# Performance work log

Hardware: AMD Instinct MI355X
Metric: run time of the kernel (lower is better)

The kernel has to match this reference:

```python
import jax, jax.numpy as jnp
import numpy as np

N, H, T, L, D_IN, D_QK, D_V = 8, 8, 1024, 1024, 128, 128, 128


def setup_inputs() -> dict:
    key = jax.random.key(0)
    ks = jax.random.split(key, 12)
    s = 1.0 / np.sqrt(D_IN)
    sq = 1.0 / np.sqrt(D_QK)
    return {
        "X": jax.random.normal(ks[0], (N, H, L, D_IN), jnp.float32),
        "t1": jax.random.normal(ks[1], (N, T), jnp.float32),
        "Q": jax.random.normal(ks[2], (N, H, T, D_QK), jnp.float32),
        "Wk1": jax.random.normal(ks[3], (D_IN, D_QK), jnp.float32) * s,
        "bk1": jnp.zeros((D_QK,), jnp.float32),
        "Wk2": jax.random.normal(ks[4], (D_QK, D_QK), jnp.float32) * sq,
        "bk2": jnp.zeros((D_QK,), jnp.float32),
        "Wv1": jax.random.normal(ks[5], (D_IN, D_QK), jnp.float32) * s,
        "bv1": jnp.zeros((D_QK,), jnp.float32),
        "Wv2": jax.random.normal(ks[6], (D_QK, D_V), jnp.float32) * sq,
        "bv2": jnp.zeros((D_V,), jnp.float32),
        "log_tau": jnp.asarray(0.0, jnp.float32),  # log(init_tau=1)
    }


def _mlp(x, W1, b1, W2, b2):
    # MLP(d_in, [d_qk], d_out): Linear -> relu -> Linear
    return jax.nn.relu(x @ W1 + b1) @ W2 + b2


def reference(X, t1, Q, Wk1, bk1, Wk2, bk2, Wv1, bv1, Wv2, bv2, log_tau):
    t2 = X[:, 0, :, -1]                      # (N, L)
    K = _mlp(X, Wk1, bk1, Wk2, bk2)          # (N, H, L, d_qk)
    V = _mlp(X, Wv1, bv1, Wv2, bv2)          # (N, H, L, d_v)
    tau = jnp.exp(log_tau)
    # gaussian weight: -(Q.K)^2 / tau
    A = jnp.einsum('nhtc,nhlc->nhtl', Q, K)
    A = -(A * A) / tau
    mask = (t1[:, :, None] >= t2[:, None, :])[:, None, :, :]  # (N,1,T,L)
    A = jax.nn.softmax(A * mask, axis=-1) * mask
    return jnp.einsum('nhtl,nhlc->nhtc', A, V)
```

## Files before the change

### kernel.cpp

```cpp
#include <hip/hip_runtime.h>
#include <hip/hip_bf16.h>

typedef __bf16 bf16_t;
typedef _Float16 f16_t;
typedef bf16_t bf16x8 __attribute__((ext_vector_type(8)));
typedef f16_t  f16x8  __attribute__((ext_vector_type(8)));
typedef float  floatx4 __attribute__((ext_vector_type(4)));
typedef bf16x8 bf16x8u __attribute__((aligned(8)));

#define DEV static __device__ __forceinline__

DEV floatx4 mfma_bf16(bf16x8 a, bf16x8 b, floatx4 c) {
  return __builtin_amdgcn_mfma_f32_16x16x32_bf16(a, b, c, 0, 0, 0);
}
DEV floatx4 mfma_f16(f16x8 a, f16x8 b, floatx4 c) {
  return __builtin_amdgcn_mfma_f32_16x16x32_f16(a, b, c, 0, 0, 0);
}
DEV void async_ld16(void* lds, const void* g) {
  __builtin_amdgcn_global_load_lds(
      (const __attribute__((address_space(1))) unsigned int*)g,
      (__attribute__((address_space(3))) unsigned int*)lds, 16, 0, 0);
}

__global__ void prep_kernel(const float* __restrict__ Wk1, const float* __restrict__ Wk2,
                            const float* __restrict__ Wv1, const float* __restrict__ Wv2,
                            const float* __restrict__ X,
                            bf16_t* __restrict__ W1p, bf16_t* __restrict__ W2p,
                            f16_t* __restrict__ W1f, f16_t* __restrict__ W2f,
                            float* __restrict__ t2pre) {
  int b = blockIdx.x;
  if (b < 16) {
    int m = b >> 2, p = b & 3;
    const float* src = m == 0 ? Wk1 : m == 1 ? Wk2 : m == 2 ? Wv1 : Wv2;
    for (int u = 0; u < 16; ++u) {
      int idx = p * 4096 + u * 256 + threadIdx.x;
      int k = idx >> 7, nn = idx & 127;
      float v = src[idx];
      int o = nn * 128 + k;
      if (m == 0) { bf16_t h = (bf16_t)v; W1p[o] = h; W1p[16384 + o] = (bf16_t)(v - (float)h); }
      else if (m == 1) { bf16_t h = (bf16_t)v; W2p[o] = h; W2p[16384 + o] = (bf16_t)(v - (float)h); }
      else if (m == 2) W1f[o] = (f16_t)v;
      else W2f[o] = (f16_t)v;
    }
  } else {
    int i = (b - 16) * 256 + threadIdx.x;
    t2pre[i] = X[((size_t)(i >> 10) * 8192 + (i & 1023)) * 128 + 127];
  }
}

__global__ __launch_bounds__(256) void mlp_k_kernel(
    const float* __restrict__ X, const float* __restrict__ b1,
    const float* __restrict__ b2, const bf16_t* __restrict__ W1p,
    const bf16_t* __restrict__ W2p, bf16_t* __restrict__ Khi,
    bf16_t* __restrict__ Klo) {
  __shared__ __align__(16) bf16_t sXh[64 * 132];
  __shared__ __align__(16) bf16_t sXl[64 * 132];
  __shared__ __align__(16) bf16_t sW[256 * 40];

  const int tid = threadIdx.x, lane = tid & 63, wave = tid >> 6;
  const int q = lane >> 4, c15 = lane & 15;
  const size_t rowBase = (size_t)blockIdx.x * 64;
  const floatx4 FZ = {0.f, 0.f, 0.f, 0.f};

  int goff[5];
  for (int a = 0; a < 5; ++a) {
    int o = (wave + 4 * a) * 1024 + lane * 16;
    int row = o / 80, rem = o % 80;
    goff[a] = row * 256 + (rem < 64 ? rem : 0);
  }
  float b1v[8], b2v[8];
  for (int nt = 0; nt < 8; ++nt) { b1v[nt] = b1[nt * 16 + c15]; b2v[nt] = b2[nt * 16 + c15]; }

  for (int u = 0; u < 8; ++u) {
    int idx = tid + u * 256;
    int r = idx >> 5, c4 = (idx & 31) << 2;
    float4 v = *(const float4*)(X + (rowBase + r) * 128 + c4);
    int o = r * 132 + c4;
    float vv[4] = {v.x, v.y, v.z, v.w};
    for (int i = 0; i < 4; ++i) {
      bf16_t h = (bf16_t)vv[i];
      sXh[o + i] = h;
      sXl[o + i] = (bf16_t)(vv[i] - (float)h);
    }
  }

  auto issueW = [&](const bf16_t* Wp, int kq) {
    const char* base = (const char*)Wp + kq * 64;
    for (int a = 0; a < 5; ++a)
      async_ld16((char*)sW + (wave + 4 * a) * 1024 + lane * 16, base + goff[a]);
  };
  auto gemm = [&](const bf16_t* Wp, floatx4* acc, bool first) {
    for (int kq = 0; kq < 4; ++kq) {
      if (!first || kq) __syncthreads();
      issueW(Wp, kq);
      __syncthreads();
      const int ao = (wave * 16 + c15) * 132 + kq * 32 + q * 8;
      bf16x8 ah = *(const bf16x8u*)(sXh + ao);
      bf16x8 al = *(const bf16x8u*)(sXl + ao);
      for (int nt = 0; nt < 8; ++nt) {
        const int bo = (nt * 16 + c15) * 40 + q * 8;
        bf16x8 bh = *(const bf16x8*)(sW + bo);
        bf16x8 bl = *(const bf16x8*)(sW + 128 * 40 + bo);
        acc[nt] = mfma_bf16(ah, bh, acc[nt]);
        acc[nt] = mfma_bf16(ah, bl, acc[nt]);
        acc[nt] = mfma_bf16(al, bh, acc[nt]);
      }
    }
  };

  floatx4 acc1[8];
  for (int i = 0; i < 8; ++i) acc1[i] = FZ;
  gemm(W1p, acc1, true);

  for (int nt = 0; nt < 8; ++nt)
    for (int r = 0; r < 4; ++r) {
      float h = fmaxf(acc1[nt][r] + b1v[nt], 0.f);
      bf16_t hh = (bf16_t)h;
      int o = (wave * 16 + q * 4 + r) * 132 + nt * 16 + c15;
      sXh[o] = hh;
      sXl[o] = (bf16_t)(h - (float)hh);
    }

  floatx4 acc2[8];
  for (int i = 0; i < 8; ++i) acc2[i] = FZ;
  gemm(W2p, acc2, false);

  for (int nt = 0; nt < 8; ++nt)
    for (int r = 0; r < 4; ++r) {
      float kv = acc2[nt][r] + b2v[nt];
      bf16_t kh = (bf16_t)kv;
      int o = (wave * 16 + q * 4 + r) * 132 + nt * 16 + c15;
      sXh[o] = kh;
      sXl[o] = (bf16_t)(kv - (float)kh);
    }
  __syncthreads();
  for (int u = 0; u < 4; ++u) {
    int idx = tid + u * 256;
    int r = idx >> 4, c8 = (idx & 15) << 3;
    bf16x8 vh = *(const bf16x8u*)(sXh + r * 132 + c8);
    bf16x8 vl = *(const bf16x8u*)(sXl + r * 132 + c8);
    *(bf16x8*)(Khi + (rowBase + r) * 128 + c8) = vh;
    *(bf16x8*)(Klo + (rowBase + r) * 128 + c8) = vl;
  }
}

__global__ __launch_bounds__(256) void mlp_v_kernel(
    const float* __restrict__ X, const float* __restrict__ b1,
    const float* __restrict__ b2, const f16_t* __restrict__ W1f,
    const f16_t* __restrict__ W2f, f16_t* __restrict__ Vt) {
  __shared__ __align__(16) f16_t sXf[9216];
  __shared__ __align__(16) f16_t sW[128 * 40];

  const int tid = threadIdx.x, lane = tid & 63, wave = tid >> 6;
  const int q = lane >> 4, c15 = lane & 15;
  const size_t rowBase = (size_t)blockIdx.x * 64;
  const floatx4 FZ = {0.f, 0.f, 0.f, 0.f};

  int goff[3];
  for (int a = 0; a < 3; ++a) {
    int j = wave + 4 * a;
    int o = j * 1024 + lane * 16;
    int row = o / 80, rem = o % 80;
    goff[a] = row * 256 + (rem < 64 ? rem : 0);
  }
  float b1v[8], bvv[2][4];
  for (int nt = 0; nt < 8; ++nt) b1v[nt] = b1[nt * 16 + c15];
  for (int mt = 0; mt < 2; ++mt)
    for (int r = 0; r < 4; ++r)
      bvv[mt][r] = b2[(wave * 2 + mt) * 16 + q * 4 + r];

  for (int u = 0; u < 8; ++u) {
    int idx = tid + u * 256;
    int r = idx >> 5, c4 = (idx & 31) << 2;
    float4 v = *(const float4*)(X + (rowBase + r) * 128 + c4);
    int o = r * 136 + c4;
    sXf[o + 0] = (f16_t)v.x; sXf[o + 1] = (f16_t)v.y;
    sXf[o + 2] = (f16_t)v.z; sXf[o + 3] = (f16_t)v.w;
  }

  auto issueV = [&](const f16_t* Wp, int kq) {
    const char* base = (const char*)Wp + kq * 64;
    for (int a = 0; a < 3; ++a) {
      int j = wave + 4 * a;
      if (j < 10) async_ld16((char*)sW + j * 1024 + lane * 16, base + goff[a]);
    }
  };

  floatx4 acc1[8];
  for (int i = 0; i < 8; ++i) acc1[i] = FZ;
  for (int kq = 0; kq < 4; ++kq) {
    if (kq) __syncthreads();
    issueV(W1f, kq);
    __syncthreads();
    f16x8 a = *(const f16x8*)(sXf + (wave * 16 + c15) * 136 + kq * 32 + q * 8);
    for (int nt = 0; nt < 8; ++nt) {
      f16x8 bb = *(const f16x8*)(sW + (nt * 16 + c15) * 40 + q * 8);
      acc1[nt] = mfma_f16(a, bb, acc1[nt]);
    }
  }
  for (int nt = 0; nt < 8; ++nt)
    for (int r = 0; r < 4; ++r)
      sXf[(wave * 16 + q * 4 + r) * 136 + nt * 16 + c15] =
          (f16_t)fmaxf(acc1[nt][r] + b1v[nt], 0.f);

  floatx4 acc2[2][4];
  for (int i = 0; i < 2; ++i) for (int j = 0; j < 4; ++j) acc2[i][j] = FZ;
  for (int kq = 0; kq < 4; ++kq) {
    __syncthreads();
    issueV(W2f, kq);
    __syncthreads();
    f16x8 aw0 = *(const f16x8*)(sW + ((wave * 2 + 0) * 16 + c15) * 40 + q * 8);
    f16x8 aw1 = *(const f16x8*)(sW + ((wave * 2 + 1) * 16 + c15) * 40 + q * 8);
    for (int nt = 0; nt < 4; ++nt) {
      f16x8 bh = *(const f16x8*)(sXf + (nt * 16 + c15) * 136 + kq * 32 + q * 8);
      acc2[0][nt] = mfma_f16(aw0, bh, acc2[0][nt]);
      acc2[1][nt] = mfma_f16(aw1, bh, acc2[1][nt]);
    }
  }
  __syncthreads();
  for (int mt = 0; mt < 2; ++mt)
    for (int nt = 0; nt < 4; ++nt)
      for (int r = 0; r < 4; ++r) {
        int c = (wave * 2 + mt) * 16 + q * 4 + r;
        sXf[c * 72 + nt * 16 + c15] = (f16_t)(acc2[mt][nt][r] + bvv[mt][r]);
      }
  __syncthreads();
  const int nh = (int)(rowBase >> 10);
  const int lB = (int)(rowBase & 1023);
  for (int u = 0; u < 4; ++u) {
    int idx = tid + u * 256;
    int c = idx >> 3, l8 = (idx & 7) << 3;
    *(f16x8*)(Vt + ((size_t)nh * 128 + c) * 1024 + lB + l8) =
        *(const f16x8*)(sXf + c * 72 + l8);
  }
}

__global__ __launch_bounds__(256) void attn_kernel(
    const float* __restrict__ Q, const float* __restrict__ t1,
    const float* __restrict__ t2pre, const float* __restrict__ ltau,
    const bf16_t* __restrict__ Khi, const bf16_t* __restrict__ Klo,
    const f16_t* __restrict__ Vt, float* __restrict__ out) {
  __shared__ __align__(16) char sBuf[2][27648];
  __shared__ __align__(16) f16_t sP[128 * 40];

  const int tid = threadIdx.x, lane = tid & 63, wave = tid >> 6;
  const int q = lane >> 4, c15 = lane & 15;
  const int nh = blockIdx.x & 63;
  const int tB = (blockIdx.x >> 6) << 7;
  const int n = nh >> 3;
  const float c2 = __expf(-ltau[0]) * 1.44269504f;
  const floatx4 FZ = {0.f, 0.f, 0.f, 0.f};

  const char* gp[7]; int ls[7]; int st[7];
  for (int a = 0; a < 7; ++a) {
    int j = wave + 4 * a;
    gp[a] = nullptr; ls[a] = 0; st[a] = 0;
    if (j < 17) {
      int o = j * 1024 + lane * 16;
      int half = o >= 8704 ? 1 : 0;
      int r2 = o - half * 8704;
      int row = r2 / 272, rem = r2 % 272;
      if (rem >= 256) rem = 0;
      gp[a] = (const char*)(half ? Klo : Khi) + ((size_t)((nh << 10) + row)) * 256 + rem;
      st[a] = 8192; ls[a] = o;
    } else if (j < 27) {
      int o = (j - 17) * 1024 + lane * 16;
      int c = o / 80, rem = o % 80;
      if (rem >= 64) rem = 0;
      gp[a] = (const char*)Vt + ((size_t)((nh << 7) + c)) * 2048 + rem;
      st[a] = 64; ls[a] = 17408 + o;
    }
  }
  auto stage = [&](int buf) {
    for (int a = 0; a < 7; ++a) {
      int j = wave + 4 * a;
      if (j < 27) { async_ld16(sBuf[buf] + ls[a], gp[a]); gp[a] += st[a]; }
    }
  };

  bf16x8 qh[2][4], ql[2][4];
  for (int mt = 0; mt < 2; ++mt) {
    int t = tB + (wave * 2 + mt) * 16 + c15;
    const float* qr = Q + ((size_t)(nh << 10) + t) * 128;
    for (int kc = 0; kc < 4; ++kc) {
      const float* p = qr + kc * 32 + q * 8;
      float4 v0 = *(const float4*)p;
      float4 v1 = *(const float4*)(p + 4);
      float vv[8] = {v0.x, v0.y, v0.z, v0.w, v1.x, v1.y, v1.z, v1.w};
      bf16x8 h, l;
      for (int j = 0; j < 8; ++j) {
        bf16_t hj = (bf16_t)vv[j];
        h[j] = hj;
        l[j] = (bf16_t)(vv[j] - (float)hj);
      }
      qh[mt][kc] = h;
      ql[mt][kc] = l;
    }
  }
  float t1v[2][4];
  for (int mt = 0; mt < 2; ++mt)
    for (int r = 0; r < 4; ++r)
      t1v[mt][r] = t1[(n << 10) + tB + (wave * 2 + mt) * 16 + q * 4 + r];
  const float* t2p = t2pre + (n << 10);

  floatx4 O[2][8];
  for (int i = 0; i < 2; ++i) for (int j = 0; j < 8; ++j) O[i][j] = FZ;
  float ds[2][4] = {{0.f, 0.f, 0.f, 0.f}, {0.f, 0.f, 0.f, 0.f}};

  stage(0);
  __syncthreads();
  for (int it = 0; it < 32; ++it) {
    const int cur = it & 1;
    if (it < 31) stage(cur ^ 1);
    float t2a = t2p[c15], t2b = t2p[c15 + 16];
    t2p += 32;
    const bf16_t* kb = (const bf16_t*)sBuf[cur];
    const f16_t* vb = (const f16_t*)(sBuf[cur] + 17408);

    floatx4 S[2][2];
    S[0][0] = FZ; S[0][1] = FZ; S[1][0] = FZ; S[1][1] = FZ;
    for (int nt = 0; nt < 2; ++nt)
      for (int kc = 0; kc < 4; ++kc) {
        int bo = (nt * 16 + c15) * 136 + kc * 32 + q * 8;
        bf16x8 bh = *(const bf16x8*)(kb + bo);
        bf16x8 bl = *(const bf16x8*)(kb + 4352 + bo);
        for (int mt = 0; mt < 2; ++mt) {
          S[mt][nt] = mfma_bf16(qh[mt][kc], bh, S[mt][nt]);
          S[mt][nt] = mfma_bf16(qh[mt][kc], bl, S[mt][nt]);
          S[mt][nt] = mfma_bf16(ql[mt][kc], bh, S[mt][nt]);
        }
      }
    for (int mt = 0; mt < 2; ++mt)
      for (int nt = 0; nt < 2; ++nt) {
        float t2v = nt ? t2b : t2a;
        for (int r = 0; r < 4; ++r) {
          float s = S[mt][nt][r];
          float e = exp2f(-s * s * c2);
          bool m = (t1v[mt][r] >= t2v);
          ds[mt][r] += m ? e : 1.f;
          sP[((wave * 2 + mt) * 16 + q * 4 + r) * 40 + nt * 16 + c15] =
              (f16_t)(m ? e : 0.f);
        }
      }
    f16x8 ap[2];
    for (int mt = 0; mt < 2; ++mt)
      ap[mt] = *(const f16x8*)(sP + ((wave * 2 + mt) * 16 + c15) * 40 + q * 8);
    for (int ct = 0; ct < 8; ++ct) {
      f16x8 bv = *(const f16x8*)(vb + (ct * 16 + c15) * 40 + q * 8);
      for (int mt = 0; mt < 2; ++mt)
        O[mt][ct] = mfma_f16(ap[mt], bv, O[mt][ct]);
    }
    __syncthreads();
  }

  for (int mt = 0; mt < 2; ++mt)
    for (int r = 0; r < 4; ++r) {
      float v = ds[mt][r];
      v += __shfl_xor(v, 1);
      v += __shfl_xor(v, 2);
      v += __shfl_xor(v, 4);
      v += __shfl_xor(v, 8);
      ds[mt][r] = 1.f / v;
    }
  for (int mt = 0; mt < 2; ++mt) {
    int rowb = tB + (wave * 2 + mt) * 16 + q * 4;
    for (int ct = 0; ct < 8; ++ct)
      for (int r = 0; r < 4; ++r)
        out[((size_t)(nh << 10) + rowb + r) * 128 + ct * 16 + c15] =
            O[mt][ct][r] * ds[mt][r];
  }
}

extern "C" void kernel_launch(void* const* d_in, const int* in_sizes, int n_in,
                              void* d_out, int out_size, void* d_ws, size_t ws_size,
                              hipStream_t stream) {
  const float* X   = (const float*)d_in[0];
  const float* t1  = (const float*)d_in[1];
  const float* Q   = (const float*)d_in[2];
  const float* Wk1 = (const float*)d_in[3];
  const float* bk1 = (const float*)d_in[4];
  const float* Wk2 = (const float*)d_in[5];
  const float* bk2 = (const float*)d_in[6];
  const float* Wv1 = (const float*)d_in[7];
  const float* bv1 = (const float*)d_in[8];
  const float* Wv2 = (const float*)d_in[9];
  const float* bv2 = (const float*)d_in[10];
  const float* log_tau = (const float*)d_in[11];
  float* out = (float*)d_out;

  const size_t E = (size_t)64 * 1024 * 128;
  bf16_t* Khi = (bf16_t*)d_ws;
  bf16_t* Klo = Khi + E;
  f16_t*  Vt  = (f16_t*)(Klo + E);
  bf16_t* W1p = (bf16_t*)((char*)d_ws + 3 * E * 2);
  bf16_t* W2p = W1p + 32768;
  f16_t*  W1f = (f16_t*)(W2p + 32768);
  f16_t*  W2f = W1f + 16384;
  float*  t2pre = (float*)(W2f + 16384);

  prep_kernel<<<48, 256, 0, stream>>>(Wk1, Wk2, Wv1, Wv2, X, W1p, W2p, W1f, W2f, t2pre);
  mlp_k_kernel<<<1024, 256, 0, stream>>>(X, bk1, bk2, W1p, W2p, Khi, Klo);
  mlp_v_kernel<<<1024, 256, 0, stream>>>(X, bv1, bv2, W1f, W2f, Vt);
  attn_kernel<<<512, 256, 0, stream>>>(Q, t1, t2pre, log_tau, Khi, Klo, Vt, out);
}
```

Measured before the change: 242.8 us.

## Rework attention to 32x32 MFMA and double-buffer MLP weights with split-bf16 V path

The attention kernel now uses 32x32 MFMA tiles, with one query row per lane. The softmax probabilities are fed straight from registers into the PV MFMA, which removes the sP shared-memory round trip and its layout. t2 is staged in LDS once, and the kernel declares a launch bound of two blocks per CU. Both MLP kernels double-buffer the weight tiles across the two GEMM phases to drop a barrier per step. The V MLP switches from fp16 to three-pass split bf16 for accuracy, which adds MFMA work and larger LDS use.

```diff
diff --git a/kernel.cpp b/kernel.cpp
--- a/kernel.cpp
+++ b/kernel.cpp
@@ -5,16 +5,21 @@
 typedef _Float16 f16_t;
 typedef bf16_t bf16x8 __attribute__((ext_vector_type(8)));
 typedef f16_t  f16x8  __attribute__((ext_vector_type(8)));
+typedef f16_t  f16x4  __attribute__((ext_vector_type(4)));
 typedef float  floatx4 __attribute__((ext_vector_type(4)));
+typedef float  floatx16 __attribute__((ext_vector_type(16)));
 typedef bf16x8 bf16x8u __attribute__((aligned(8)));
 
 #define DEV static __device__ __forceinline__
 
-DEV floatx4 mfma_bf16(bf16x8 a, bf16x8 b, floatx4 c) {
+DEV floatx4 mfma16_bf16(bf16x8 a, bf16x8 b, floatx4 c) {
   return __builtin_amdgcn_mfma_f32_16x16x32_bf16(a, b, c, 0, 0, 0);
 }
-DEV floatx4 mfma_f16(f16x8 a, f16x8 b, floatx4 c) {
-  return __builtin_amdgcn_mfma_f32_16x16x32_f16(a, b, c, 0, 0, 0);
+DEV floatx16 mfma32_bf16(bf16x8 a, bf16x8 b, floatx16 c) {
+  return __builtin_amdgcn_mfma_f32_32x32x16_bf16(a, b, c, 0, 0, 0);
+}
+DEV floatx16 mfma32x8_f16(f16x4 a, f16x4 b, floatx16 c) {
+  return __builtin_amdgcn_mfma_f32_32x32x8f16(a, b, c, 0, 0, 0);
 }
 DEV void async_ld16(void* lds, const void* g) {
   __builtin_amdgcn_global_load_lds(
@@ -26,21 +31,21 @@
                             const float* __restrict__ Wv1, const float* __restrict__ Wv2,
                             const float* __restrict__ X,
                             bf16_t* __restrict__ W1p, bf16_t* __restrict__ W2p,
-                            f16_t* __restrict__ W1f, f16_t* __restrict__ W2f,
+                            bf16_t* __restrict__ W3p, bf16_t* __restrict__ W4p,
                             float* __restrict__ t2pre) {
   int b = blockIdx.x;
   if (b < 16) {
     int m = b >> 2, p = b & 3;
     const float* src = m == 0 ? Wk1 : m == 1 ? Wk2 : m == 2 ? Wv1 : Wv2;
+    bf16_t* dst = m == 0 ? W1p : m == 1 ? W2p : m == 2 ? W3p : W4p;
     for (int u = 0; u < 16; ++u) {
       int idx = p * 4096 + u * 256 + threadIdx.x;
       int k = idx >> 7, nn = idx & 127;
       float v = src[idx];
       int o = nn * 128 + k;
-      if (m == 0) { bf16_t h = (bf16_t)v; W1p[o] = h; W1p[16384 + o] = (bf16_t)(v - (float)h); }
-      else if (m == 1) { bf16_t h = (bf16_t)v; W2p[o] = h; W2p[16384 + o] = (bf16_t)(v - (float)h); }
-      else if (m == 2) W1f[o] = (f16_t)v;
-      else W2f[o] = (f16_t)v;
+      bf16_t h = (bf16_t)v;
+      dst[o] = h;
+      dst[16384 + o] = (bf16_t)(v - (float)h);
     }
   } else {
     int i = (b - 16) * 256 + threadIdx.x;
@@ -53,14 +58,14 @@
     const float* __restrict__ b2, const bf16_t* __restrict__ W1p,
     const bf16_t* __restrict__ W2p, bf16_t* __restrict__ Khi,
     bf16_t* __restrict__ Klo) {
-  __shared__ __align__(16) bf16_t sXh[64 * 132];
-  __shared__ __align__(16) bf16_t sXl[64 * 132];
-  __shared__ __align__(16) bf16_t sW[256 * 40];
+  __shared__ __align__(16) char sXbuf[2 * 16896];
+  __shared__ __align__(16) bf16_t sW[2][256 * 40];
+  bf16_t* sXh = (bf16_t*)sXbuf;
+  bf16_t* sXl = sXh + 64 * 132;
 
   const int tid = threadIdx.x, lane = tid & 63, wave = tid >> 6;
   const int q = lane >> 4, c15 = lane & 15;
   const size_t rowBase = (size_t)blockIdx.x * 64;
-  const floatx4 FZ = {0.f, 0.f, 0.f, 0.f};
 
   int goff[5];
   for (int a = 0; a < 5; ++a) {
@@ -84,46 +89,47 @@
     }
   }
 
-  auto issueW = [&](const bf16_t* Wp, int kq) {
-    const char* base = (const char*)Wp + kq * 64;
+  auto issueW = [&](int buf, int ph) {
+    const bf16_t* Wp = (ph < 4) ? W1p : W2p;
+    const char* base = (const char*)Wp + (ph & 3) * 64;
     for (int a = 0; a < 5; ++a)
-      async_ld16((char*)sW + (wave + 4 * a) * 1024 + lane * 16, base + goff[a]);
+      async_ld16((char*)sW[buf] + (wave + 4 * a) * 1024 + lane * 16, base + goff[a]);
   };
-  auto gemm = [&](const bf16_t* Wp, floatx4* acc, bool first) {
-    for (int kq = 0; kq < 4; ++kq) {
-      if (!first || kq) __syncthreads();
-      issueW(Wp, kq);
-      __syncthreads();
-      const int ao = (wave * 16 + c15) * 132 + kq * 32 + q * 8;
-      bf16x8 ah = *(const bf16x8u*)(sXh + ao);
-      bf16x8 al = *(const bf16x8u*)(sXl + ao);
-      for (int nt = 0; nt < 8; ++nt) {
-        const int bo = (nt * 16 + c15) * 40 + q * 8;
-        bf16x8 bh = *(const bf16x8*)(sW + bo);
-        bf16x8 bl = *(const bf16x8*)(sW + 128 * 40 + bo);
-        acc[nt] = mfma_bf16(ah, bh, acc[nt]);
-        acc[nt] = mfma_bf16(ah, bl, acc[nt]);
-        acc[nt] = mfma_bf16(al, bh, acc[nt]);
-      }
-    }
-  };
-
-  floatx4 acc1[8];
-  for (int i = 0; i < 8; ++i) acc1[i] = FZ;
-  gemm(W1p, acc1, true);
-
-  for (int nt = 0; nt < 8; ++nt)
-    for (int r = 0; r < 4; ++r) {
-      float h = fmaxf(acc1[nt][r] + b1v[nt], 0.f);
-      bf16_t hh = (bf16_t)h;
-      int o = (wave * 16 + q * 4 + r) * 132 + nt * 16 + c15;
-      sXh[o] = hh;
-      sXl[o] = (bf16_t)(h - (float)hh);
-    }
-
-  floatx4 acc2[8];
-  for (int i = 0; i < 8; ++i) acc2[i] = FZ;
-  gemm(W2p, acc2, false);
+
+  floatx4 acc1[8], acc2[8];
+  for (int i = 0; i < 8; ++i) { acc1[i] = {}; acc2[i] = {}; }
+
+  issueW(0, 0);
+  __syncthreads();
+#pragma unroll
+  for (int ph = 0; ph < 8; ++ph) {
+    if (ph < 7) issueW((ph + 1) & 1, ph + 1);
+    const bf16_t* wb = sW[ph & 1];
+    const int kq = ph & 3;
+    floatx4* acc = (ph < 4) ? acc1 : acc2;
+    const int ao = (wave * 16 + c15) * 132 + kq * 32 + q * 8;
+    bf16x8 ah = *(const bf16x8u*)(sXh + ao);
+    bf16x8 al = *(const bf16x8u*)(sXl + ao);
+    for (int nt = 0; nt < 8; ++nt) {
+      const int bo = (nt * 16 + c15) * 40 + q * 8;
+      bf16x8 bh = *(const bf16x8*)(wb + bo);
+      bf16x8 bl = *(const bf16x8*)(wb + 128 * 40 + bo);
+      acc[nt] = mfma16_bf16(ah, bh, acc[nt]);
+      acc[nt] = mfma16_bf16(ah, bl, acc[nt]);
+      acc[nt] = mfma16_bf16(al, bh, acc[nt]);
+    }
+    if (ph == 3) {
+      for (int nt = 0; nt < 8; ++nt)
+        for (int r = 0; r < 4; ++r) {
+          float h = fmaxf(acc1[nt][r] + b1v[nt], 0.f);
+          bf16_t hh = (bf16_t)h;
+          int o = (wave * 16 + q * 4 + r) * 132 + nt * 16 + c15;
+          sXh[o] = hh;
+          sXl[o] = (bf16_t)(h - (float)hh);
+        }
+    }
+    __syncthreads();
+  }
 
   for (int nt = 0; nt < 8; ++nt)
     for (int r = 0; r < 4; ++r) {
@@ -146,20 +152,20 @@
 
 __global__ __launch_bounds__(256) void mlp_v_kernel(
     const float* __restrict__ X, const float* __restrict__ b1,
-    const float* __restrict__ b2, const f16_t* __restrict__ W1f,
-    const f16_t* __restrict__ W2f, f16_t* __restrict__ Vt) {
-  __shared__ __align__(16) f16_t sXf[9216];
-  __shared__ __align__(16) f16_t sW[128 * 40];
+    const float* __restrict__ b2, const bf16_t* __restrict__ W1p,
+    const bf16_t* __restrict__ W2p, f16_t* __restrict__ Vt) {
+  __shared__ __align__(16) char sXbuf[2 * 16896];
+  __shared__ __align__(16) bf16_t sW[2][256 * 40];
+  bf16_t* sXh = (bf16_t*)sXbuf;
+  bf16_t* sXl = sXh + 64 * 132;
 
   const int tid = threadIdx.x, lane = tid & 63, wave = tid >> 6;
   const int q = lane >> 4, c15 = lane & 15;
   const size_t rowBase = (size_t)blockIdx.x * 64;
-  const floatx4 FZ = {0.f, 0.f, 0.f, 0.f};
-
-  int goff[3];
-  for (int a = 0; a < 3; ++a) {
-    int j = wave + 4 * a;
-    int o = j * 1024 + lane * 16;
+
+  int goff[5];
+  for (int a = 0; a < 5; ++a) {
+    int o = (wave + 4 * a) * 1024 + lane * 16;
     int row = o / 80, rem = o % 80;
     goff[a] = row * 256 + (rem < 64 ? rem : 0);
   }
@@ -173,56 +179,82 @@
     int idx = tid + u * 256;
     int r = idx >> 5, c4 = (idx & 31) << 2;
     float4 v = *(const float4*)(X + (rowBase + r) * 128 + c4);
-    int o = r * 136 + c4;
-    sXf[o + 0] = (f16_t)v.x; sXf[o + 1] = (f16_t)v.y;
-    sXf[o + 2] = (f16_t)v.z; sXf[o + 3] = (f16_t)v.w;
-  }
-
-  auto issueV = [&](const f16_t* Wp, int kq) {
-    const char* base = (const char*)Wp + kq * 64;
-    for (int a = 0; a < 3; ++a) {
-      int j = wave + 4 * a;
-      if (j < 10) async_ld16((char*)sW + j * 1024 + lane * 16, base + goff[a]);
-    }
+    int o = r * 132 + c4;
+    float vv[4] = {v.x, v.y, v.z, v.w};
+    for (int i = 0; i < 4; ++i) {
+      bf16_t h = (bf16_t)vv[i];
+      sXh[o + i] = h;
+      sXl[o + i] = (bf16_t)(vv[i] - (float)h);
+    }
+  }
+
+  auto issueW = [&](int buf, int ph) {
+    const bf16_t* Wp = (ph < 4) ? W1p : W2p;
+    const char* base = (const char*)Wp + (ph & 3) * 64;
+    for (int a = 0; a < 5; ++a)
+      async_ld16((char*)sW[buf] + (wave + 4 * a) * 1024 + lane * 16, base + goff[a]);
   };
 
-  floatx4 acc1[8];
-  for (int i = 0; i < 8; ++i) acc1[i] = FZ;
-  for (int kq = 0; kq < 4; ++kq) {
-    if (kq) __syncthreads();
-    issueV(W1f, kq);
+  floatx4 acc1[8], acc2[2][4];
+  for (int i = 0; i < 8; ++i) acc1[i] = {};
+  for (int i = 0; i < 2; ++i) for (int j = 0; j < 4; ++j) acc2[i][j] = {};
+
+  issueW(0, 0);
+  __syncthreads();
+#pragma unroll
+  for (int ph = 0; ph < 8; ++ph) {
+    if (ph < 7) issueW((ph + 1) & 1, ph + 1);
+    const bf16_t* wb = sW[ph & 1];
+    const int kq = ph & 3;
+    if (ph < 4) {
+      const int ao = (wave * 16 + c15) * 132 + kq * 32 + q * 8;
+      bf16x8 ah = *(const bf16x8u*)(sXh + ao);
+      bf16x8 al = *(const bf16x8u*)(sXl + ao);
+      for (int nt = 0; nt < 8; ++nt) {
+        const int bo = (nt * 16 + c15) * 40 + q * 8;
+        bf16x8 bh = *(const bf16x8*)(wb + bo);
+        bf16x8 bl = *(const bf16x8*)(wb + 128 * 40 + bo);
+        acc1[nt] = mfma16_bf16(ah, bh, acc1[nt]);
+        acc1[nt] = mfma16_bf16(ah, bl, acc1[nt]);
+        acc1[nt] = mfma16_bf16(al, bh, acc1[nt]);
+      }
+      if (ph == 3) {
+        for (int nt = 0; nt < 8; ++nt)
+          for (int r = 0; r < 4; ++r) {
+            float h = fmaxf(acc1[nt][r] + b1v[nt], 0.f);
+            bf16_t hh = (bf16_t)h;
+            int o = (wave * 16 + q * 4 + r) * 132 + nt * 16 + c15;
+            sXh[o] = hh;
+            sXl[o] = (bf16_t)(h - (float)hh);
+          }
+      }
+    } else {
+      bf16x8 awh[2], awl[2];
+      for (int mt = 0; mt < 2; ++mt) {
+        const int aoo = ((wave * 2 + mt) * 16 + c15) * 40 + q * 8;
+        awh[mt] = *(const bf16x8*)(wb + aoo);
+        awl[mt] = *(const bf16x8*)(wb + 128 * 40 + aoo);
+      }
+      for (int nt = 0; nt < 4; ++nt) {
+        const int bo = (nt * 16 + c15) * 132 + kq * 32 + q * 8;
+        bf16x8 bh = *(const bf16x8u*)(sXh + bo);
+        bf16x8 bl = *(const bf16x8u*)(sXl + bo);
+        for (int mt = 0; mt < 2; ++mt) {
+          acc2[mt][nt] = mfma16_bf16(awh[mt], bh, acc2[mt][nt]);
+          acc2[mt][nt] = mfma16_bf16(awh[mt], bl, acc2[mt][nt]);
+          acc2[mt][nt] = mfma16_bf16(awl[mt], bh, acc2[mt][nt]);
+        }
+      }
+    }
     __syncthreads();
-    f16x8 a = *(const f16x8*)(sXf + (wave * 16 + c15) * 136 + kq * 32 + q * 8);
-    for (int nt = 0; nt < 8; ++nt) {
-      f16x8 bb = *(const f16x8*)(sW + (nt * 16 + c15) * 40 + q * 8);
-      acc1[nt] = mfma_f16(a, bb, acc1[nt]);
-    }
-  }
-  for (int nt = 0; nt < 8; ++nt)
-    for (int r = 0; r < 4; ++r)
-      sXf[(wave * 16 + q * 4 + r) * 136 + nt * 16 + c15] =
-          (f16_t)fmaxf(acc1[nt][r] + b1v[nt], 0.f);
-
-  floatx4 acc2[2][4];
-  for (int i = 0; i < 2; ++i) for (int j = 0; j < 4; ++j) acc2[i][j] = FZ;
-  for (int kq = 0; kq < 4; ++kq) {
-    __syncthreads();
-    issueV(W2f, kq);
-    __syncthreads();
-    f16x8 aw0 = *(const f16x8*)(sW + ((wave * 2 + 0) * 16 + c15) * 40 + q * 8);
-    f16x8 aw1 = *(const f16x8*)(sW + ((wave * 2 + 1) * 16 + c15) * 40 + q * 8);
-    for (int nt = 0; nt < 4; ++nt) {
-      f16x8 bh = *(const f16x8*)(sXf + (nt * 16 + c15) * 136 + kq * 32 + q * 8);
-      acc2[0][nt] = mfma_f16(aw0, bh, acc2[0][nt]);
-      acc2[1][nt] = mfma_f16(aw1, bh, acc2[1][nt]);
-    }
-  }
-  __syncthreads();
+  }
+
+  f16_t* sVT = (f16_t*)sXbuf;
   for (int mt = 0; mt < 2; ++mt)
     for (int nt = 0; nt < 4; ++nt)
       for (int r = 0; r < 4; ++r) {
         int c = (wave * 2 + mt) * 16 + q * 4 + r;
-        sXf[c * 72 + nt * 16 + c15] = (f16_t)(acc2[mt][nt][r] + bvv[mt][r]);
+        sVT[c * 72 + nt * 16 + c15] = (f16_t)(acc2[mt][nt][r] + bvv[mt][r]);
       }
   __syncthreads();
   const int nh = (int)(rowBase >> 10);
@@ -231,25 +263,25 @@
     int idx = tid + u * 256;
     int c = idx >> 3, l8 = (idx & 7) << 3;
     *(f16x8*)(Vt + ((size_t)nh * 128 + c) * 1024 + lB + l8) =
-        *(const f16x8*)(sXf + c * 72 + l8);
-  }
-}
-
-__global__ __launch_bounds__(256) void attn_kernel(
+        *(const f16x8*)(sVT + c * 72 + l8);
+  }
+}
+
+__global__ __launch_bounds__(256, 2) void attn_kernel(
     const float* __restrict__ Q, const float* __restrict__ t1,
     const float* __restrict__ t2pre, const float* __restrict__ ltau,
     const bf16_t* __restrict__ Khi, const bf16_t* __restrict__ Klo,
     const f16_t* __restrict__ Vt, float* __restrict__ out) {
   __shared__ __align__(16) char sBuf[2][27648];
-  __shared__ __align__(16) f16_t sP[128 * 40];
+  __shared__ __align__(16) float sT2[1024];
 
   const int tid = threadIdx.x, lane = tid & 63, wave = tid >> 6;
-  const int q = lane >> 4, c15 = lane & 15;
+  const int h = lane >> 5, l31 = lane & 31;
   const int nh = blockIdx.x & 63;
   const int tB = (blockIdx.x >> 6) << 7;
   const int n = nh >> 3;
+  const int qrow = tB + wave * 32 + l31;
   const float c2 = __expf(-ltau[0]) * 1.44269504f;
-  const floatx4 FZ = {0.f, 0.f, 0.f, 0.f};
 
   const char* gp[7]; int ls[7]; int st[7];
   for (int a = 0; a < 7; ++a) {
@@ -278,97 +310,80 @@
     }
   };
 
-  bf16x8 qh[2][4], ql[2][4];
-  for (int mt = 0; mt < 2; ++mt) {
-    int t = tB + (wave * 2 + mt) * 16 + c15;
-    const float* qr = Q + ((size_t)(nh << 10) + t) * 128;
-    for (int kc = 0; kc < 4; ++kc) {
-      const float* p = qr + kc * 32 + q * 8;
+  stage(0);
+  *(float4*)(sT2 + tid * 4) = *(const float4*)(t2pre + (n << 10) + tid * 4);
+
+  bf16x8 qh[8], ql[8];
+  {
+    const float* qr = Q + ((size_t)(nh << 10) + qrow) * 128;
+    for (int ks = 0; ks < 8; ++ks) {
+      const float* p = qr + ks * 16 + h * 8;
       float4 v0 = *(const float4*)p;
       float4 v1 = *(const float4*)(p + 4);
       float vv[8] = {v0.x, v0.y, v0.z, v0.w, v1.x, v1.y, v1.z, v1.w};
-      bf16x8 h, l;
+      bf16x8 hi, lo;
       for (int j = 0; j < 8; ++j) {
         bf16_t hj = (bf16_t)vv[j];
-        h[j] = hj;
-        l[j] = (bf16_t)(vv[j] - (float)hj);
-      }
-      qh[mt][kc] = h;
-      ql[mt][kc] = l;
-    }
-  }
-  float t1v[2][4];
-  for (int mt = 0; mt < 2; ++mt)
-    for (int r = 0; r < 4; ++r)
-      t1v[mt][r] = t1[(n << 10) + tB + (wave * 2 + mt) * 16 + q * 4 + r];
-  const float* t2p = t2pre + (n << 10);
-
-  floatx4 O[2][8];
-  for (int i = 0; i < 2; ++i) for (int j = 0; j < 8; ++j) O[i][j] = FZ;
-  float ds[2][4] = {{0.f, 0.f, 0.f, 0.f}, {0.f, 0.f, 0.f, 0.f}};
-
-  stage(0);
+        hi[j] = hj;
+        lo[j] = (bf16_t)(vv[j] - (float)hj);
+      }
+      qh[ks] = hi;
+      ql[ks] = lo;
+    }
+  }
+  const float t1v = t1[(n << 10) + qrow];
+
+  floatx16 O[4];
+  for (int i = 0; i < 4; ++i) O[i] = {};
+  float ds = 0.f;
+
   __syncthreads();
   for (int it = 0; it < 32; ++it) {
     const int cur = it & 1;
     if (it < 31) stage(cur ^ 1);
-    float t2a = t2p[c15], t2b = t2p[c15 + 16];
-    t2p += 32;
-    const bf16_t* kb = (const bf16_t*)sBuf[cur];
-    const f16_t* vb = (const f16_t*)(sBuf[cur] + 17408);
-
-    floatx4 S[2][2];
-    S[0][0] = FZ; S[0][1] = FZ; S[1][0] = FZ; S[1][1] = FZ;
-    for (int nt = 0; nt < 2; ++nt)
-      for (int kc = 0; kc < 4; ++kc) {
-        int bo = (nt * 16 + c15) * 136 + kc * 32 + q * 8;
-        bf16x8 bh = *(const bf16x8*)(kb + bo);
-        bf16x8 bl = *(const bf16x8*)(kb + 4352 + bo);
-        for (int mt = 0; mt < 2; ++mt) {
-          S[mt][nt] = mfma_bf16(qh[mt][kc], bh, S[mt][nt]);
-          S[mt][nt] = mfma_bf16(qh[mt][kc], bl, S[mt][nt]);
-          S[mt][nt] = mfma_bf16(ql[mt][kc], bh, S[mt][nt]);
-        }
-      }
-    for (int mt = 0; mt < 2; ++mt)
-      for (int nt = 0; nt < 2; ++nt) {
-        float t2v = nt ? t2b : t2a;
-        for (int r = 0; r < 4; ++r) {
-          float s = S[mt][nt][r];
-          float e = exp2f(-s * s * c2);
-          bool m = (t1v[mt][r] >= t2v);
-          ds[mt][r] += m ? e : 1.f;
-          sP[((wave * 2 + mt) * 16 + q * 4 + r) * 40 + nt * 16 + c15] =
-              (f16_t)(m ? e : 0.f);
-        }
-      }
-    f16x8 ap[2];
-    for (int mt = 0; mt < 2; ++mt)
-      ap[mt] = *(const f16x8*)(sP + ((wave * 2 + mt) * 16 + c15) * 40 + q * 8);
-    for (int ct = 0; ct < 8; ++ct) {
-      f16x8 bv = *(const f16x8*)(vb + (ct * 16 + c15) * 40 + q * 8);
-      for (int mt = 0; mt < 2; ++mt)
-        O[mt][ct] = mfma_f16(ap[mt], bv, O[mt][ct]);
+    const char* kb = sBuf[cur];
+    const char* vb = sBuf[cur] + 17408;
+
+    floatx16 S = {};
+    for (int ks = 0; ks < 8; ++ks) {
+      const int bo = l31 * 272 + ks * 32 + h * 16;
+      bf16x8 kh_ = *(const bf16x8*)(kb + bo);
+      bf16x8 kl_ = *(const bf16x8*)(kb + 8704 + bo);
+      S = mfma32_bf16(kh_, qh[ks], S);
+      S = mfma32_bf16(kl_, qh[ks], S);
+      S = mfma32_bf16(kh_, ql[ks], S);
+    }
+
+    const float* t2b = sT2 + it * 32 + h * 4;
+    for (int t = 0; t < 4; ++t) {
+      float4 t2v = *(const float4*)(t2b + t * 8);
+      float tv[4] = {t2v.x, t2v.y, t2v.z, t2v.w};
+      f16x4 pb;
+      for (int j = 0; j < 4; ++j) {
+        float s = S[4 * t + j];
+        float e = exp2f(-s * s * c2);
+        bool m = (t1v >= tv[j]);
+        ds += m ? e : 1.f;
+        pb[j] = (f16_t)(m ? e : 0.f);
+      }
+      for (int ct = 0; ct < 4; ++ct) {
+        f16x4 va = *(const f16x4*)(vb + (ct * 32 + l31) * 80 + t * 16 + h * 8);
+        O[ct] = mfma32x8_f16(va, pb, O[ct]);
+      }
     }
     __syncthreads();
   }
 
-  for (int mt = 0; mt < 2; ++mt)
-    for (int r = 0; r < 4; ++r) {
-      float v = ds[mt][r];
-      v += __shfl_xor(v, 1);
-      v += __shfl_xor(v, 2);
-      v += __shfl_xor(v, 4);
-      v += __shfl_xor(v, 8);
-      ds[mt][r] = 1.f / v;
-    }
-  for (int mt = 0; mt < 2; ++mt) {
-    int rowb = tB + (wave * 2 + mt) * 16 + q * 4;
-    for (int ct = 0; ct < 8; ++ct)
-      for (int r = 0; r < 4; ++r)
-        out[((size_t)(nh << 10) + rowb + r) * 128 + ct * 16 + c15] =
-            O[mt][ct][r] * ds[mt][r];
-  }
+  ds += __shfl_xor(ds, 32);
+  const float inv = 1.f / ds;
+  float* orow = out + ((size_t)(nh << 10) + qrow) * 128;
+  for (int ct = 0; ct < 4; ++ct)
+    for (int t = 0; t < 4; ++t) {
+      int c = ct * 32 + 8 * t + 4 * h;
+      float4 v = {O[ct][4 * t + 0] * inv, O[ct][4 * t + 1] * inv,
+                  O[ct][4 * t + 2] * inv, O[ct][4 * t + 3] * inv};
+      *(float4*)(orow + c) = v;
+    }
 }
 
 extern "C" void kernel_launch(void* const* d_in, const int* in_sizes, int n_in,
@@ -394,12 +409,12 @@
   f16_t*  Vt  = (f16_t*)(Klo + E);
   bf16_t* W1p = (bf16_t*)((char*)d_ws + 3 * E * 2);
   bf16_t* W2p = W1p + 32768;
-  f16_t*  W1f = (f16_t*)(W2p + 32768);
-  f16_t*  W2f = W1f + 16384;
-  float*  t2pre = (float*)(W2f + 16384);
-
-  prep_kernel<<<48, 256, 0, stream>>>(Wk1, Wk2, Wv1, Wv2, X, W1p, W2p, W1f, W2f, t2pre);
+  bf16_t* W3p = W2p + 32768;
+  bf16_t* W4p = W3p + 32768;
+  float*  t2pre = (float*)(W4p + 32768);
+
+  prep_kernel<<<48, 256, 0, stream>>>(Wk1, Wk2, Wv1, Wv2, X, W1p, W2p, W3p, W4p, t2pre);
   mlp_k_kernel<<<1024, 256, 0, stream>>>(X, bk1, bk2, W1p, W2p, Khi, Klo);
-  mlp_v_kernel<<<1024, 256, 0, stream>>>(X, bv1, bv2, W1f, W2f, Vt);
+  mlp_v_kernel<<<1024, 256, 0, stream>>>(X, bv1, bv2, W3p, W4p, Vt);
   attn_kernel<<<512, 256, 0, stream>>>(Q, t1, t2pre, log_tau, Khi, Klo, Vt, out);
 }
```

After: 250.2 us. 1.03x slower.
